# Kernel optimization log

Measured on AMD Instinct MI355X. Metric: run time of the kernel, lower is better.

The kernel has to match this reference:

```python
import jax, jax.numpy as jnp
import numpy as np

V, N, K, D, H = 100000, 20000, 32, 256, 256


def setup_inputs() -> dict:
    key = jax.random.key(0)
    k1, k2, k3, k4, k5, k6 = jax.random.split(key, 6)
    return {
        "embed_table": jax.random.normal(k1, (V, D), dtype=jnp.float32),
        "node_ids": jax.random.randint(k2, (N,), 0, V, dtype=jnp.int64) if jax.config.jax_enable_x64 else jax.random.randint(k2, (N,), 0, V, dtype=jnp.int32),
        "nb_ids": jax.random.randint(k3, (N, K), 0, V, dtype=jnp.int32),
        "self_weight": jax.random.normal(k4, (D, H), dtype=jnp.float32) / np.sqrt(D),
        "nb_weight": jax.random.normal(k5, (D, H), dtype=jnp.float32) / np.sqrt(D),
        "bias": jax.random.normal(k6, (2 * H,), dtype=jnp.float32),
    }


def reference(embed_table, node_ids, nb_ids, self_weight, nb_weight, bias):
    # gather self embeddings: [N, D]
    self_attr = embed_table[node_ids]
    # gather sampled neighbor embeddings [N, K, D] and mean-pool over K
    nb_attr = jnp.mean(embed_table[nb_ids], axis=1)
    from_self = self_attr @ self_weight          # [N, H]
    from_nb = nb_attr @ nb_weight                # [N, H]
    out = jnp.concatenate((from_self, from_nb), axis=1) + bias  # concat combine
    return jax.nn.relu(out)
```

## Files before the change

kernel.cpp:

```cpp
#include <hip/hip_runtime.h>

#define VV 100000
#define NN 20000
#define KK 32
#define DD 256
#define HH 256
#define BN 16

typedef __attribute__((ext_vector_type(8))) short bf16x8;
typedef __attribute__((ext_vector_type(4))) float f32x4;
typedef __attribute__((ext_vector_type(2))) float f32x2;
typedef __attribute__((ext_vector_type(4))) uint  u32x4;
typedef __attribute__((ext_vector_type(2))) uint  u32x2;

__device__ __forceinline__ ushort f2bf(float f) {
    uint u = __float_as_uint(f);
    return (ushort)((u + 0x7FFFu + ((u >> 16) & 1u)) >> 16);
}
__device__ __forceinline__ float bf2f(ushort u) {
    return __uint_as_float(((uint)u) << 16);
}

__global__ __launch_bounds__(256) void k_conv8(
    const float* __restrict__ E, unsigned char* __restrict__ E8)
{
    const size_t i = ((size_t)blockIdx.x * 256 + threadIdx.x) * 16;
    u32x4 o;
    #pragma unroll
    for (int w = 0; w < 4; ++w) {
        const f32x4 a = __builtin_nontemporal_load((const f32x4*)&E[i + w * 4]);
        int r = 0;
        r = __builtin_amdgcn_cvt_pk_fp8_f32(a.x, a.y, r, false);
        r = __builtin_amdgcn_cvt_pk_fp8_f32(a.z, a.w, r, true);
        o[w] = (uint)r;
    }
    *(u32x4*)&E8[i] = o;
}

__global__ __launch_bounds__(256) void k_conv(
    const float* __restrict__ E, ushort* __restrict__ Eb)
{
    const size_t i = ((size_t)blockIdx.x * 256 + threadIdx.x) * 8;
    const f32x4 a = __builtin_nontemporal_load((const f32x4*)&E[i]);
    const f32x4 b = __builtin_nontemporal_load((const f32x4*)&E[i + 4]);
    bf16x8 v;
    v[0] = (short)f2bf(a.x); v[1] = (short)f2bf(a.y);
    v[2] = (short)f2bf(a.z); v[3] = (short)f2bf(a.w);
    v[4] = (short)f2bf(b.x); v[5] = (short)f2bf(b.y);
    v[6] = (short)f2bf(b.z); v[7] = (short)f2bf(b.w);
    *(bf16x8*)&Eb[i] = v;
}

__global__ __launch_bounds__(256) void k_prep_wf(
    const float* __restrict__ Ws, const float* __restrict__ Wn,
    ushort* __restrict__ WTf)
{
    __shared__ float t[256][17];
    const int tid = threadIdx.x;
    const int h   = blockIdx.y;
    const int tt  = blockIdx.x;
    const float* src = h ? Wn : Ws;
    const int h0 = tt * 16;
    const int c = tid & 15, dr = tid >> 4;
    #pragma unroll
    for (int s = 0; s < 16; ++s) {
        const int d = s * 16 + dr;
        t[d][c] = src[(size_t)d * HH + h0 + c];
    }
    __syncthreads();
    const int fl = tid & 63, w = tid >> 6;
    const int r16 = fl & 15, kg = fl >> 4;
    #pragma unroll
    for (int p = 0; p < 2; ++p) {
        const int ks = w + p * 4;
        bf16x8 v;
        #pragma unroll
        for (int e = 0; e < 8; ++e)
            v[e] = (short)f2bf(t[ks * 32 + kg * 8 + e][r16]);
        *(bf16x8*)&WTf[(((size_t)(h * 16 + tt) * 8 + ks) * 64 + fl) * 8] = v;
    }
}

__global__ __launch_bounds__(256) void k_prep_w(
    const float* __restrict__ Ws, const float* __restrict__ Wn,
    ushort* __restrict__ WT)
{
    __shared__ float t[64][65];
    const int tid = threadIdx.x;
    const float* src = (blockIdx.z == 0) ? Ws : Wn;
    ushort* dst = WT + (size_t)blockIdx.z * HH * DD;
    const int d0 = blockIdx.x * 64, h0 = blockIdx.y * 64;

    const int hl = tid & 63, dq = tid >> 6;
    #pragma unroll
    for (int i = 0; i < 16; ++i) {
        const int dl = dq * 16 + i;
        t[dl][hl] = src[(size_t)(d0 + dl) * HH + h0 + hl];
    }
    __syncthreads();
    const int dl = tid & 63, hq = tid >> 6;
    #pragma unroll
    for (int i = 0; i < 16; ++i) {
        const int h2 = hq * 16 + i;
        dst[(size_t)(h0 + h2) * DD + d0 + dl] = f2bf(t[dl][h2]);
    }
}

__global__ __launch_bounds__(256, 4) void k_gather8(
    const float*         __restrict__ Ef,
    const unsigned char* __restrict__ E8,
    const int*           __restrict__ node_ids,
    const int*           __restrict__ nb_ids,
    ushort*              __restrict__ A)
{
    const int wv   = threadIdx.x >> 6;
    const int lane = threadIdx.x & 63;
    const int sub  = lane >> 5, l31 = lane & 31;
    const int g    = blockIdx.x * 4 + wv;
    const int base = g * KK;

    const int srow = node_ids[g];
    const f32x4 s0 = *(const f32x4*)&Ef[(size_t)(uint)srow * DD + l31 * 8];
    const f32x4 s1 = *(const f32x4*)&Ef[(size_t)(uint)srow * DD + l31 * 8 + 4];

    u32x2 d[16];
    #pragma unroll
    for (int j = 0; j < 16; ++j) {
        const int rlo = nb_ids[base + 2 * j];
        const int rhi = nb_ids[base + 2 * j + 1];
        const int row = sub ? rhi : rlo;
        d[j] = *(const u32x2*)&E8[(size_t)(uint)row * DD + l31 * 8];
    }

    float acc[8];
    #pragma unroll
    for (int e = 0; e < 8; ++e) acc[e] = 0.f;
    #pragma unroll
    for (int j = 0; j < 16; ++j) {
        #pragma unroll
        for (int w = 0; w < 2; ++w) {
            const f32x2 lo = __builtin_amdgcn_cvt_pk_f32_fp8((int)d[j][w], false);
            const f32x2 hi = __builtin_amdgcn_cvt_pk_f32_fp8((int)d[j][w], true);
            acc[w * 4 + 0] += lo.x; acc[w * 4 + 1] += lo.y;
            acc[w * 4 + 2] += hi.x; acc[w * 4 + 3] += hi.y;
        }
    }
    #pragma unroll
    for (int e = 0; e < 8; ++e)
        acc[e] += __shfl_xor(acc[e], 32);

    const float inv = 1.0f / (float)KK;
    bf16x8 nv;
    #pragma unroll
    for (int e = 0; e < 8; ++e)
        nv[e] = (short)f2bf(acc[e] * inv);

    bf16x8 sv;
    sv[0] = (short)f2bf(s0.x); sv[1] = (short)f2bf(s0.y);
    sv[2] = (short)f2bf(s0.z); sv[3] = (short)f2bf(s0.w);
    sv[4] = (short)f2bf(s1.x); sv[5] = (short)f2bf(s1.y);
    sv[6] = (short)f2bf(s1.z); sv[7] = (short)f2bf(s1.w);

    const int tile = g >> 4, rr = g & 15;
    const int ks = l31 >> 2, kgw = l31 & 3;
    const size_t dst = (((size_t)(tile * 2 + sub) * 8 + ks) * 64 + kgw * 16 + rr) * 8;
    *(bf16x8*)&A[dst] = sub ? nv : sv;
}

__global__ __launch_bounds__(256, 4) void k_gemmf(
    const ushort* __restrict__ A,
    const ushort* __restrict__ WTf,
    const float*  __restrict__ bias,
    float*        __restrict__ out)
{
    const int wv   = __builtin_amdgcn_readfirstlane((int)(threadIdx.x >> 6));
    const int lane = threadIdx.x & 63;
    const int tile = blockIdx.x;
    const int half = wv >> 1, qt = wv & 1;
    const int r16 = lane & 15, kg = lane >> 4;

    bf16x8 a[8];
    #pragma unroll
    for (int ks = 0; ks < 8; ++ks)
        a[ks] = *(const bf16x8*)&A[(((size_t)(tile * 2 + half) * 8 + ks) * 64 + lane) * 8];

    f32x4 accs[8];
    #pragma unroll
    for (int ct = 0; ct < 8; ++ct) {
        const int t = qt * 8 + ct;
        f32x4 acc = {0.f, 0.f, 0.f, 0.f};
        #pragma unroll
        for (int ks = 0; ks < 8; ++ks) {
            const bf16x8 b = *(const bf16x8*)&WTf[(((size_t)(half * 16 + t) * 8 + ks) * 64 + lane) * 8];
            acc = __builtin_amdgcn_mfma_f32_16x16x32_bf16(a[ks], b, acc, 0, 0, 0);
        }
        accs[ct] = acc;
    }

    #pragma unroll
    for (int ct = 0; ct < 8; ++ct) {
        const int cglob = half * HH + (qt * 8 + ct) * 16 + r16;
        const float bv = bias[cglob];
        #pragma unroll
        for (int r = 0; r < 4; ++r) {
            const float v = accs[ct][r] + bv;
            out[(size_t)(tile * 16 + kg * 4 + r) * (2 * HH) + cglob] = v > 0.f ? v : 0.f;
        }
    }
}

template<int EBF16>
__global__ __launch_bounds__(256, 4) void k_fused(
    const float*  __restrict__ Ef,
    const ushort* __restrict__ Eb,
    const int*    __restrict__ node_ids,
    const int*    __restrict__ nb_ids,
    const ushort* __restrict__ WT,
    const float*  __restrict__ bias,
    float*        __restrict__ out)
{
    __shared__ ushort As[BN][DD];
    __shared__ ushort An[BN][DD];
    const int tid  = threadIdx.x;
    const int wave = tid >> 6;
    const int lane = tid & 63;
    const int g0   = blockIdx.x * BN;

    if (EBF16) {
        const int sub = lane >> 5;
        const int l31 = lane & 31;
        const uint boff = (uint)l31 * 16;
        for (int n = wave; n < BN; n += 4) {
            const int g = g0 + n;
            const int base = g * KK;
            const uint swz = ((uint)(n & 7)) << 4;
            const int srow = node_ids[g];
            const bf16x8 sv = *(const bf16x8*)&Eb[((size_t)(uint)srow << 8) + l31 * 8];
            bf16x8 r[16];
            #pragma unroll
            for (int j = 0; j < 16; ++j) {
                const int rlo = nb_ids[base + 2 * j];
                const int rhi = nb_ids[base + 2 * j + 1];
                const int row = sub ? rhi : rlo;
                r[j] = *(const bf16x8*)&Eb[((size_t)(uint)row << 8) + l31 * 8];
            }
            float acc[8];
            #pragma unroll
            for (int e = 0; e < 8; ++e) acc[e] = 0.f;
            #pragma unroll
            for (int j = 0; j < 16; ++j) {
                #pragma unroll
                for (int e = 0; e < 8; ++e)
                    acc[e] += bf2f((ushort)r[j][e]);
            }
            #pragma unroll
            for (int e = 0; e < 8; ++e)
                acc[e] += __shfl_xor(acc[e], 32);
            const float inv = 1.0f / (float)KK;
            bf16x8 nv;
            #pragma unroll
            for (int e = 0; e < 8; ++e)
                nv[e] = (short)f2bf(acc[e] * inv);
            if (sub == 0) {
                *(bf16x8*)((char*)&As[n][0] + (boff ^ swz)) = sv;
            } else {
                *(bf16x8*)((char*)&An[n][0] + (boff ^ swz)) = nv;
            }
        }
    } else {
        for (int n = wave; n < BN; n += 4) {
            const int g = g0 + n;
            const int srow = node_ids[g];
            const uint swz  = ((uint)(n & 7)) << 4;
            const uint boff = (uint)lane * 8;
            const float4 s = *(const float4*)&Ef[(size_t)srow * DD + lane * 4];
            ushort4 sv = make_ushort4(f2bf(s.x), f2bf(s.y), f2bf(s.z), f2bf(s.w));
            float4 acc = make_float4(0.f, 0.f, 0.f, 0.f);
            #pragma unroll
            for (int k0 = 0; k0 < KK; k0 += 8) {
                float4 r[8];
                #pragma unroll
                for (int j = 0; j < 8; ++j) {
                    const int row = nb_ids[g * KK + k0 + j];
                    r[j] = *(const float4*)&Ef[(size_t)row * DD + lane * 4];
                }
                #pragma unroll
                for (int j = 0; j < 8; ++j) {
                    acc.x += r[j].x; acc.y += r[j].y;
                    acc.z += r[j].z; acc.w += r[j].w;
                }
            }
            const float inv = 1.0f / (float)KK;
            const ushort4 nv = make_ushort4(f2bf(acc.x * inv), f2bf(acc.y * inv),
                                            f2bf(acc.z * inv), f2bf(acc.w * inv));
            *(ushort4*)((char*)&As[n][0] + (boff ^ swz)) = sv;
            *(ushort4*)((char*)&An[n][0] + (boff ^ swz)) = nv;
        }
    }
    __syncthreads();

    const int half = wave >> 1;
    const int colq = (wave & 1) * 128;
    const int r16  = lane & 15;
    const int kg   = lane >> 4;
    const uint rswz = ((uint)(r16 & 7)) << 4;
    const char* Arow = (const char*)(half ? &An[r16][0] : &As[r16][0]);

    bf16x8 a[8];
    #pragma unroll
    for (int ks = 0; ks < 8; ++ks) {
        const uint off = (uint)(ks * 64 + kg * 16);
        a[ks] = *(const bf16x8*)(Arow + (off ^ rswz));
    }

    const ushort* Wb = WT + (size_t)half * HH * DD;
    f32x4 accs[8];
    #pragma unroll
    for (int ct = 0; ct < 8; ++ct) {
        const int c = colq + ct * 16 + r16;
        const ushort* Bb = Wb + (size_t)c * DD + kg * 8;
        f32x4 acc = {0.f, 0.f, 0.f, 0.f};
        #pragma unroll
        for (int ks = 0; ks < 8; ++ks) {
            const bf16x8 b = *(const bf16x8*)(Bb + ks * 32);
            acc = __builtin_amdgcn_mfma_f32_16x16x32_bf16(a[ks], b, acc, 0, 0, 0);
        }
        accs[ct] = acc;
    }

    #pragma unroll
    for (int ct = 0; ct < 8; ++ct) {
        const int cglob = half * HH + colq + ct * 16 + r16;
        const float bv = bias[cglob];
        #pragma unroll
        for (int r = 0; r < 4; ++r) {
            const float v = accs[ct][r] + bv;
            out[(size_t)(g0 + kg * 4 + r) * (2 * HH) + cglob] = v > 0.f ? v : 0.f;
        }
    }
}

__global__ __launch_bounds__(256, 4) void hetegraph_fused_kernel(
    const float* __restrict__ embed, const int* __restrict__ node_ids,
    const int* __restrict__ nb_ids, const float* __restrict__ Ws,
    const float* __restrict__ Wn, const float* __restrict__ bias,
    float* __restrict__ out)
{
    __shared__ float As[BN][DD];
    __shared__ float An[BN][DD];
    const int tid = threadIdx.x, wave = tid >> 6, lane = tid & 63;
    const int g0 = blockIdx.x * BN;
    for (int n = wave; n < BN; n += 4) {
        const int g = g0 + n;
        const int self_row = node_ids[g];
        const float4 s = *(const float4*)&embed[(size_t)self_row * DD + lane * 4];
        float4 acc = make_float4(0.f, 0.f, 0.f, 0.f);
        for (int k0 = 0; k0 < KK; k0 += 8) {
            float4 r[8];
            #pragma unroll
            for (int j = 0; j < 8; ++j) {
                const int row = nb_ids[g * KK + k0 + j];
                r[j] = *(const float4*)&embed[(size_t)row * DD + lane * 4];
            }
            #pragma unroll
            for (int j = 0; j < 8; ++j) {
                acc.x += r[j].x; acc.y += r[j].y; acc.z += r[j].z; acc.w += r[j].w;
            }
        }
        const float inv = 1.0f / (float)KK;
        *(float4*)&As[n][lane * 4] = s;
        float4 m = make_float4(acc.x * inv, acc.y * inv, acc.z * inv, acc.w * inv);
        *(float4*)&An[n][lane * 4] = m;
    }
    __syncthreads();
    const int h = tid;
    {
        float acc[BN];
        #pragma unroll
        for (int n = 0; n < BN; ++n) acc[n] = 0.f;
        for (int d0 = 0; d0 < DD; d0 += 4) {
            const float w0 = Ws[(d0+0)*HH+h], w1 = Ws[(d0+1)*HH+h];
            const float w2 = Ws[(d0+2)*HH+h], w3 = Ws[(d0+3)*HH+h];
            #pragma unroll
            for (int n = 0; n < BN; ++n) {
                const float4 a = *(const float4*)&As[n][d0];
                acc[n] = fmaf(a.x,w0,acc[n]); acc[n] = fmaf(a.y,w1,acc[n]);
                acc[n] = fmaf(a.z,w2,acc[n]); acc[n] = fmaf(a.w,w3,acc[n]);
            }
        }
        const float b = bias[h];
        #pragma unroll
        for (int n = 0; n < BN; ++n) {
            const float v = acc[n] + b;
            out[(size_t)(g0+n)*(2*HH) + h] = v > 0.f ? v : 0.f;
        }
    }
    {
        float acc[BN];
        #pragma unroll
        for (int n = 0; n < BN; ++n) acc[n] = 0.f;
        for (int d0 = 0; d0 < DD; d0 += 4) {
            const float w0 = Wn[(d0+0)*HH+h], w1 = Wn[(d0+1)*HH+h];
            const float w2 = Wn[(d0+2)*HH+h], w3 = Wn[(d0+3)*HH+h];
            #pragma unroll
            for (int n = 0; n < BN; ++n) {
                const float4 a = *(const float4*)&An[n][d0];
                acc[n] = fmaf(a.x,w0,acc[n]); acc[n] = fmaf(a.y,w1,acc[n]);
                acc[n] = fmaf(a.z,w2,acc[n]); acc[n] = fmaf(a.w,w3,acc[n]);
            }
        }
        const float b = bias[HH + h];
        #pragma unroll
        for (int n = 0; n < BN; ++n) {
            const float v = acc[n] + b;
            out[(size_t)(g0+n)*(2*HH) + HH + h] = v > 0.f ? v : 0.f;
        }
    }
}

extern "C" void kernel_launch(void* const* d_in, const int* in_sizes, int n_in,
                              void* d_out, int out_size, void* d_ws, size_t ws_size,
                              hipStream_t stream) {
    const float* embed    = (const float*)d_in[0];
    const int*   node_ids = (const int*)d_in[1];
    const int*   nb_ids   = (const int*)d_in[2];
    const float* Ws       = (const float*)d_in[3];
    const float* Wn       = (const float*)d_in[4];
    const float* bias     = (const float*)d_in[5];
    float*       out      = (float*)d_out;

    const size_t e8_bytes  = (size_t)VV * DD;
    const size_t eb_bytes  = (size_t)VV * DD * sizeof(ushort);
    const size_t wtf_bytes = 2ull * 16 * 8 * 64 * 8 * sizeof(ushort);
    const size_t af_bytes  = (size_t)(NN / 16) * 2 * 8 * 64 * 8 * sizeof(ushort);
    const size_t wt_bytes  = 2ull * HH * DD * sizeof(ushort);

    if (ws_size >= e8_bytes + wtf_bytes + af_bytes) {
        unsigned char* E8  = (unsigned char*)d_ws;
        ushort*        WTf = (ushort*)((char*)d_ws + e8_bytes);
        ushort*        Af  = (ushort*)((char*)d_ws + e8_bytes + wtf_bytes);
        k_prep_wf<<<dim3(16, 2), dim3(256), 0, stream>>>(Ws, Wn, WTf);
        k_conv8<<<dim3(VV * DD / 4096), dim3(256), 0, stream>>>(embed, E8);
        k_gather8<<<dim3(NN / 4), dim3(256), 0, stream>>>(embed, E8, node_ids, nb_ids, Af);
        k_gemmf<<<dim3(NN / 16), dim3(256), 0, stream>>>(Af, WTf, bias, out);
    } else if (ws_size >= eb_bytes + wt_bytes) {
        ushort* Eb = (ushort*)d_ws;
        ushort* WT = (ushort*)((char*)d_ws + eb_bytes);
        k_conv<<<dim3(VV * DD / 2048), dim3(256), 0, stream>>>(embed, Eb);
        k_prep_w<<<dim3(DD / 64, HH / 64, 2), dim3(256), 0, stream>>>(Ws, Wn, WT);
        k_fused<1><<<dim3(NN / BN), dim3(256), 0, stream>>>(
            nullptr, Eb, node_ids, nb_ids, WT, bias, out);
    } else if (ws_size >= wt_bytes) {
        ushort* WT = (ushort*)d_ws;
        k_prep_w<<<dim3(DD / 64, HH / 64, 2), dim3(256), 0, stream>>>(Ws, Wn, WT);
        k_fused<0><<<dim3(NN / BN), dim3(256), 0, stream>>>(
            embed, nullptr, node_ids, nb_ids, WT, bias, out);
    } else {
        hetegraph_fused_kernel<<<dim3(NN / BN), dim3(256), 0, stream>>>(
            embed, node_ids, nb_ids, Ws, Wn, bias, out);
    }
}
```

Before: 93.53 us.

## Fuse fp8 neighbor gather and MFMA GEMM into one kernel via LDS

Replaces the separate gather kernel (writing bf16 A tiles to global memory) and GEMM kernel with a single 512-thread kernel. The kernel gathers self and mean-pooled fp8 neighbor rows into XOR-swizzled shared memory, then runs the MFMA GEMM straight from LDS. It uses the plain transposed weight layout instead of the fragment-packed one. This removes the global round trip for the intermediate activations and one launch, but adds a block barrier and lowers gather parallelism per block.

```diff
diff --git a/kernel.cpp b/kernel.cpp
--- a/kernel.cpp
+++ b/kernel.cpp
@@ -51,36 +51,6 @@
     *(bf16x8*)&Eb[i] = v;
 }
 
-__global__ __launch_bounds__(256) void k_prep_wf(
-    const float* __restrict__ Ws, const float* __restrict__ Wn,
-    ushort* __restrict__ WTf)
-{
-    __shared__ float t[256][17];
-    const int tid = threadIdx.x;
-    const int h   = blockIdx.y;
-    const int tt  = blockIdx.x;
-    const float* src = h ? Wn : Ws;
-    const int h0 = tt * 16;
-    const int c = tid & 15, dr = tid >> 4;
-    #pragma unroll
-    for (int s = 0; s < 16; ++s) {
-        const int d = s * 16 + dr;
-        t[d][c] = src[(size_t)d * HH + h0 + c];
-    }
-    __syncthreads();
-    const int fl = tid & 63, w = tid >> 6;
-    const int r16 = fl & 15, kg = fl >> 4;
-    #pragma unroll
-    for (int p = 0; p < 2; ++p) {
-        const int ks = w + p * 4;
-        bf16x8 v;
-        #pragma unroll
-        for (int e = 0; e < 8; ++e)
-            v[e] = (short)f2bf(t[ks * 32 + kg * 8 + e][r16]);
-        *(bf16x8*)&WTf[(((size_t)(h * 16 + tt) * 8 + ks) * 64 + fl) * 8] = v;
-    }
-}
-
 __global__ __launch_bounds__(256) void k_prep_w(
     const float* __restrict__ Ws, const float* __restrict__ Wn,
     ushort* __restrict__ WT)
@@ -106,105 +76,118 @@
     }
 }
 
-__global__ __launch_bounds__(256, 4) void k_gather8(
+__global__ __launch_bounds__(512, 6) void k_fused8(
     const float*         __restrict__ Ef,
     const unsigned char* __restrict__ E8,
     const int*           __restrict__ node_ids,
     const int*           __restrict__ nb_ids,
-    ushort*              __restrict__ A)
-{
-    const int wv   = threadIdx.x >> 6;
-    const int lane = threadIdx.x & 63;
+    const ushort*        __restrict__ WT,
+    const float*         __restrict__ bias,
+    float*               __restrict__ out)
+{
+    __shared__ ushort As[BN][DD];
+    __shared__ ushort An[BN][DD];
+    const int tid  = threadIdx.x;
+    const int wv   = tid >> 6;
+    const int lane = tid & 63;
     const int sub  = lane >> 5, l31 = lane & 31;
-    const int g    = blockIdx.x * 4 + wv;
-    const int base = g * KK;
-
-    const int srow = node_ids[g];
-    const f32x4 s0 = *(const f32x4*)&Ef[(size_t)(uint)srow * DD + l31 * 8];
-    const f32x4 s1 = *(const f32x4*)&Ef[(size_t)(uint)srow * DD + l31 * 8 + 4];
-
-    u32x2 d[16];
-    #pragma unroll
-    for (int j = 0; j < 16; ++j) {
-        const int rlo = nb_ids[base + 2 * j];
-        const int rhi = nb_ids[base + 2 * j + 1];
-        const int row = sub ? rhi : rlo;
-        d[j] = *(const u32x2*)&E8[(size_t)(uint)row * DD + l31 * 8];
-    }
-
-    float acc[8];
-    #pragma unroll
-    for (int e = 0; e < 8; ++e) acc[e] = 0.f;
-    #pragma unroll
-    for (int j = 0; j < 16; ++j) {
-        #pragma unroll
-        for (int w = 0; w < 2; ++w) {
-            const f32x2 lo = __builtin_amdgcn_cvt_pk_f32_fp8((int)d[j][w], false);
-            const f32x2 hi = __builtin_amdgcn_cvt_pk_f32_fp8((int)d[j][w], true);
-            acc[w * 4 + 0] += lo.x; acc[w * 4 + 1] += lo.y;
-            acc[w * 4 + 2] += hi.x; acc[w * 4 + 3] += hi.y;
-        }
-    }
-    #pragma unroll
-    for (int e = 0; e < 8; ++e)
-        acc[e] += __shfl_xor(acc[e], 32);
-
-    const float inv = 1.0f / (float)KK;
-    bf16x8 nv;
-    #pragma unroll
-    for (int e = 0; e < 8; ++e)
-        nv[e] = (short)f2bf(acc[e] * inv);
-
-    bf16x8 sv;
-    sv[0] = (short)f2bf(s0.x); sv[1] = (short)f2bf(s0.y);
-    sv[2] = (short)f2bf(s0.z); sv[3] = (short)f2bf(s0.w);
-    sv[4] = (short)f2bf(s1.x); sv[5] = (short)f2bf(s1.y);
-    sv[6] = (short)f2bf(s1.z); sv[7] = (short)f2bf(s1.w);
-
-    const int tile = g >> 4, rr = g & 15;
-    const int ks = l31 >> 2, kgw = l31 & 3;
-    const size_t dst = (((size_t)(tile * 2 + sub) * 8 + ks) * 64 + kgw * 16 + rr) * 8;
-    *(bf16x8*)&A[dst] = sub ? nv : sv;
-}
-
-__global__ __launch_bounds__(256, 4) void k_gemmf(
-    const ushort* __restrict__ A,
-    const ushort* __restrict__ WTf,
-    const float*  __restrict__ bias,
-    float*        __restrict__ out)
-{
-    const int wv   = __builtin_amdgcn_readfirstlane((int)(threadIdx.x >> 6));
-    const int lane = threadIdx.x & 63;
-    const int tile = blockIdx.x;
-    const int half = wv >> 1, qt = wv & 1;
-    const int r16 = lane & 15, kg = lane >> 4;
+    const int g0   = blockIdx.x * BN;
+
+    #pragma unroll
+    for (int it = 0; it < 2; ++it) {
+        const int n = wv + it * 8;
+        const int g = g0 + n;
+        const int base = g * KK;
+        const uint swz  = ((uint)(n & 7)) << 4;
+        const uint boff = (uint)l31 * 16;
+
+        const int srow = node_ids[g];
+        const f32x4 s0 = *(const f32x4*)&Ef[(size_t)(uint)srow * DD + l31 * 8];
+        const f32x4 s1 = *(const f32x4*)&Ef[(size_t)(uint)srow * DD + l31 * 8 + 4];
+
+        u32x2 d[16];
+        #pragma unroll
+        for (int j = 0; j < 16; ++j) {
+            const int rlo = nb_ids[base + 2 * j];
+            const int rhi = nb_ids[base + 2 * j + 1];
+            const int row = sub ? rhi : rlo;
+            d[j] = *(const u32x2*)&E8[(size_t)(uint)row * DD + l31 * 8];
+        }
+
+        float acc[8];
+        #pragma unroll
+        for (int e = 0; e < 8; ++e) acc[e] = 0.f;
+        #pragma unroll
+        for (int j = 0; j < 16; ++j) {
+            #pragma unroll
+            for (int w = 0; w < 2; ++w) {
+                const f32x2 lo = __builtin_amdgcn_cvt_pk_f32_fp8((int)d[j][w], false);
+                const f32x2 hi = __builtin_amdgcn_cvt_pk_f32_fp8((int)d[j][w], true);
+                acc[w * 4 + 0] += lo.x; acc[w * 4 + 1] += lo.y;
+                acc[w * 4 + 2] += hi.x; acc[w * 4 + 3] += hi.y;
+            }
+        }
+        #pragma unroll
+        for (int e = 0; e < 8; ++e)
+            acc[e] += __shfl_xor(acc[e], 32);
+
+        const float inv = 1.0f / (float)KK;
+        bf16x8 nv;
+        #pragma unroll
+        for (int e = 0; e < 8; ++e)
+            nv[e] = (short)f2bf(acc[e] * inv);
+
+        bf16x8 sv;
+        sv[0] = (short)f2bf(s0.x); sv[1] = (short)f2bf(s0.y);
+        sv[2] = (short)f2bf(s0.z); sv[3] = (short)f2bf(s0.w);
+        sv[4] = (short)f2bf(s1.x); sv[5] = (short)f2bf(s1.y);
+        sv[6] = (short)f2bf(s1.z); sv[7] = (short)f2bf(s1.w);
+
+        if (sub == 0) {
+            *(bf16x8*)((char*)&As[n][0] + (boff ^ swz)) = sv;
+        } else {
+            *(bf16x8*)((char*)&An[n][0] + (boff ^ swz)) = nv;
+        }
+    }
+    __syncthreads();
+
+    const int half = wv >> 2;
+    const int colo = (wv & 3) * 64;
+    const int r16  = lane & 15;
+    const int kg   = lane >> 4;
+    const uint rswz = ((uint)(r16 & 7)) << 4;
+    const char* Arow = (const char*)(half ? &An[r16][0] : &As[r16][0]);
 
     bf16x8 a[8];
     #pragma unroll
-    for (int ks = 0; ks < 8; ++ks)
-        a[ks] = *(const bf16x8*)&A[(((size_t)(tile * 2 + half) * 8 + ks) * 64 + lane) * 8];
-
-    f32x4 accs[8];
-    #pragma unroll
-    for (int ct = 0; ct < 8; ++ct) {
-        const int t = qt * 8 + ct;
+    for (int ks = 0; ks < 8; ++ks) {
+        const uint off = (uint)(ks * 64 + kg * 16);
+        a[ks] = *(const bf16x8*)(Arow + (off ^ rswz));
+    }
+
+    const ushort* Wb = WT + (size_t)half * HH * DD;
+    f32x4 accs[4];
+    #pragma unroll
+    for (int ct = 0; ct < 4; ++ct) {
+        const int c = colo + ct * 16 + r16;
+        const ushort* Bb = Wb + (size_t)c * DD + kg * 8;
         f32x4 acc = {0.f, 0.f, 0.f, 0.f};
         #pragma unroll
         for (int ks = 0; ks < 8; ++ks) {
-            const bf16x8 b = *(const bf16x8*)&WTf[(((size_t)(half * 16 + t) * 8 + ks) * 64 + lane) * 8];
+            const bf16x8 b = *(const bf16x8*)(Bb + ks * 32);
             acc = __builtin_amdgcn_mfma_f32_16x16x32_bf16(a[ks], b, acc, 0, 0, 0);
         }
         accs[ct] = acc;
     }
 
     #pragma unroll
-    for (int ct = 0; ct < 8; ++ct) {
-        const int cglob = half * HH + (qt * 8 + ct) * 16 + r16;
+    for (int ct = 0; ct < 4; ++ct) {
+        const int cglob = half * HH + colo + ct * 16 + r16;
         const float bv = bias[cglob];
         #pragma unroll
         for (int r = 0; r < 4; ++r) {
             const float v = accs[ct][r] + bv;
-            out[(size_t)(tile * 16 + kg * 4 + r) * (2 * HH) + cglob] = v > 0.f ? v : 0.f;
+            out[(size_t)(g0 + kg * 4 + r) * (2 * HH) + cglob] = v > 0.f ? v : 0.f;
         }
     }
 }
@@ -429,20 +412,17 @@
     const float* bias     = (const float*)d_in[5];
     float*       out      = (float*)d_out;
 
-    const size_t e8_bytes  = (size_t)VV * DD;
-    const size_t eb_bytes  = (size_t)VV * DD * sizeof(ushort);
-    const size_t wtf_bytes = 2ull * 16 * 8 * 64 * 8 * sizeof(ushort);
-    const size_t af_bytes  = (size_t)(NN / 16) * 2 * 8 * 64 * 8 * sizeof(ushort);
-    const size_t wt_bytes  = 2ull * HH * DD * sizeof(ushort);
-
-    if (ws_size >= e8_bytes + wtf_bytes + af_bytes) {
-        unsigned char* E8  = (unsigned char*)d_ws;
-        ushort*        WTf = (ushort*)((char*)d_ws + e8_bytes);
-        ushort*        Af  = (ushort*)((char*)d_ws + e8_bytes + wtf_bytes);
-        k_prep_wf<<<dim3(16, 2), dim3(256), 0, stream>>>(Ws, Wn, WTf);
+    const size_t e8_bytes = (size_t)VV * DD;
+    const size_t eb_bytes = (size_t)VV * DD * sizeof(ushort);
+    const size_t wt_bytes = 2ull * HH * DD * sizeof(ushort);
+
+    if (ws_size >= e8_bytes + wt_bytes) {
+        unsigned char* E8 = (unsigned char*)d_ws;
+        ushort*        WT = (ushort*)((char*)d_ws + e8_bytes);
         k_conv8<<<dim3(VV * DD / 4096), dim3(256), 0, stream>>>(embed, E8);
-        k_gather8<<<dim3(NN / 4), dim3(256), 0, stream>>>(embed, E8, node_ids, nb_ids, Af);
-        k_gemmf<<<dim3(NN / 16), dim3(256), 0, stream>>>(Af, WTf, bias, out);
+        k_prep_w<<<dim3(DD / 64, HH / 64, 2), dim3(256), 0, stream>>>(Ws, Wn, WT);
+        k_fused8<<<dim3(NN / BN), dim3(512), 0, stream>>>(
+            embed, E8, node_ids, nb_ids, WT, bias, out);
     } else if (ws_size >= eb_bytes + wt_bytes) {
         ushort* Eb = (ushort*)d_ws;
         ushort* WT = (ushort*)((char*)d_ws + eb_bytes);
```

Measured after the change: 102.7 us. 9.8% more time.
